# Kernel tuning notes

Hardware: AMD Instinct MI355X
Metric: run time of the kernel (lower is better)

The kernel has to match this reference:

```python
import jax, jax.numpy as jnp
import numpy as np

N_HEADS = 16
D_HEAD = 64
N_ROTATE = 32
ROPE_BASE = 10000.0
MAX_LEN = 2048  # round_up_to_multiple_of_256(keep count); static for jit
BATCH, SEQ = 2, 4096


def setup_inputs() -> dict:
    key = jax.random.key(0)
    kq, kk, kv = jax.random.split(key, 3)
    q = jax.random.normal(kq, (BATCH, N_HEADS, MAX_LEN, D_HEAD), jnp.float32)
    k = jax.random.normal(kk, (BATCH, N_HEADS, SEQ, D_HEAD), jnp.float32)
    v = jax.random.normal(kv, (BATCH, N_HEADS, SEQ, D_HEAD), jnp.float32)
    # causal full mask [batch, seq, seq] and full position ids [batch, seq]
    mask_full = jnp.broadcast_to(jnp.tril(jnp.ones((SEQ, SEQ), bool)), (BATCH, SEQ, SEQ))
    pos_full = jnp.broadcast_to(jnp.arange(SEQ, dtype=jnp.int32), (BATCH, SEQ))
    # skip_mask: exactly MAX_LEN kept tokens per row (random positions)
    rng = np.random.default_rng(0)
    sm = np.zeros((BATCH, SEQ), dtype=bool)
    for i in range(BATCH):
        sm[i, rng.permutation(SEQ)[:MAX_LEN]] = True
    return {"q": q, "k": k, "v": v, "mask_full": mask_full,
            "pos_full": pos_full, "skip_mask": jnp.asarray(sm)}


def _rope_rotate(x, pos):
    # x: [b, h, L, n_rotate], pos: [b, L]
    half = N_ROTATE // 2
    inv_freq = 1.0 / (ROPE_BASE ** (jnp.arange(0, N_ROTATE, 2, dtype=jnp.float32) / N_ROTATE))
    freqs = pos.astype(jnp.float32)[..., None] * inv_freq          # [b, L, half]
    emb = jnp.concatenate([freqs, freqs], axis=-1)[:, None]        # [b, 1, L, n_rotate]
    cos, sin = jnp.cos(emb), jnp.sin(emb)
    x1, x2 = x[..., :half], x[..., half:]
    rot = jnp.concatenate([-x2, x1], axis=-1)                      # rotate_half
    return x * cos + rot * sin


def reference(q, k, v, mask_full, pos_full, skip_mask):
    b, S = skip_mask.shape
    lengths = skip_mask.sum(axis=1)
    # vectorized _trim_attention_mask: stable argsort compacts kept indices to the front
    order = jnp.argsort(jnp.where(skip_mask, 0, 1), axis=1, stable=True)
    idx = order[:, :MAX_LEN]                                       # [b, max_len]
    brow = jnp.arange(b)[:, None]
    mask_trim = mask_full[brow, idx]                               # [b, max_len, S]
    pos_trim = pos_full[brow, idx]                                 # [b, max_len]
    valid = jnp.arange(MAX_LEN)[None, :] < lengths[:, None]
    mask_trim = mask_trim & valid[..., None]
    pos_trim = jnp.where(valid, pos_trim, 0)

    # partial RoPE on first n_rotate channels
    rq = _rope_rotate(q[..., :N_ROTATE], pos_trim)
    rk = _rope_rotate(k[..., :N_ROTATE], pos_full)
    q = jnp.concatenate([rq, q[..., N_ROTATE:]], axis=-1)
    k = jnp.concatenate([rk, k[..., N_ROTATE:]], axis=-1)

    # masked SDPA (bool mask broadcast over heads)
    scale = 1.0 / jnp.sqrt(jnp.float32(D_HEAD))
    scores = jnp.einsum('bhqd,bhkd->bhqk', q, k) * scale
    scores = jnp.where(mask_trim[:, None], scores, jnp.finfo(scores.dtype).min)
    attn = jax.nn.softmax(scores, axis=-1)
    return jnp.einsum('bhqk,bhkd->bhqd', attn, v)
```

## Files before the change

kernel.cpp:

```cpp
#include <hip/hip_runtime.h>
#include <math.h>

#define BB 2
#define HH 16
#define QQ 2048
#define SS 4096
#define DD 64
#define NRH 16
#define NQT 32

typedef unsigned short u16;
typedef unsigned int   u32;
typedef short bhalf8 __attribute__((ext_vector_type(8)));
typedef float f32x4  __attribute__((ext_vector_type(4)));

typedef __attribute__((address_space(1))) const u32 gu32;
typedef __attribute__((address_space(3))) u32 lu32;

#if __has_builtin(__builtin_amdgcn_exp2f)
#define EXP2(x) __builtin_amdgcn_exp2f(x)
#else
#define EXP2(x) exp2f(x)
#endif

union Frag16 { uint4 u; bhalf8 v; u16 s[8]; uint2 d[2]; };

__device__ __forceinline__ u16 f2bf(float f) {
  union { float f; u32 u; } c; c.f = f;
  return (u16)((c.u + 0x7FFFu + ((c.u >> 16) & 1u)) >> 16);
}

__device__ __forceinline__ u32 cvt_pk_bf16(float lo, float hi) {
  u32 r;
  asm("v_cvt_pk_bf16_f32 %0, %1, %2" : "=v"(r) : "v"(lo), "v"(hi));
  return r;
}

__device__ __forceinline__ bhalf8 ldfrag(const u16* p) {
  Frag16 f; f.u = *reinterpret_cast<const uint4*>(p); return f.v;
}

__device__ __forceinline__ void rope32(float* x, int pos) {
  const float step = 0.8304820237218405f;
  const float fp = (float)pos;
#pragma unroll
  for (int i = 0; i < NRH; ++i) {
    float ang = fp * exp2f(-step * (float)i);
    float sv, cv;
    __sincosf(ang, &sv, &cv);
    float a = x[i], b = x[i + NRH];
    x[i]       = a * cv - b * sv;
    x[i + NRH] = b * cv + a * sv;
  }
}

__global__ void prep_idx_kernel(const unsigned char* __restrict__ sm,
                                int* __restrict__ idx) {
  __shared__ int wsum[4];
  __shared__ int modes;
  const int tid = threadIdx.x;
  const int b = (int)blockIdx.x;

  int c = 0;
  for (int i = 0; i < 32; ++i) c += (sm[tid * 32 + i] != 0) ? 1 : 0;
#pragma unroll
  for (int off = 32; off; off >>= 1) c += __shfl_down(c, off);
  if ((tid & 63) == 0) wsum[tid >> 6] = c;
  __syncthreads();
  if (tid == 0) modes = (wsum[0] + wsum[1] + wsum[2] + wsum[3] > 3000) ? 1 : 0;
  __syncthreads();
  const bool byteMode = (modes != 0);
  const u32* sm32 = (const u32*)sm;

  const int base = b * SS + tid * 16;
  u32 flags = 0;
  for (int i = 0; i < 16; ++i) {
    bool f = byteMode ? (sm[base + i] != 0) : (sm32[base + i] != 0);
    flags |= ((u32)(f ? 1 : 0)) << i;
  }
  int cnt = __popc(flags);
  int vv = cnt;
#pragma unroll
  for (int off = 1; off < 64; off <<= 1) {
    int t = __shfl_up(vv, off);
    if ((tid & 63) >= off) vv += t;
  }
  __syncthreads();
  if ((tid & 63) == 63) wsum[tid >> 6] = vv;
  __syncthreads();
  int add = 0;
  for (int w2 = 0; w2 < (tid >> 6); ++w2) add += wsum[w2];
  int p = vv - cnt + add;
  for (int i = 0; i < 16; ++i) {
    if (flags & (1u << i)) {
      if (p < QQ) idx[b * QQ + p] = tid * 16 + i;
      ++p;
    }
  }
}

__global__ __launch_bounds__(256) void prep_kv_kernel(const float* __restrict__ k,
                                                      const float* __restrict__ v,
                                                      u16* __restrict__ kbf,
                                                      u16* __restrict__ vt) {
  __shared__ u16 tile[64][72];
  if (blockIdx.x < 512) {
    int r = blockIdx.x * 256 + threadIdx.x;
    int pos = r & (SS - 1);
    float x[64];
    const float4* src = (const float4*)(k + (size_t)r * DD);
#pragma unroll
    for (int i = 0; i < 16; ++i) {
      float4 t = src[i];
      x[4 * i] = t.x; x[4 * i + 1] = t.y; x[4 * i + 2] = t.z; x[4 * i + 3] = t.w;
    }
    rope32(x, pos);
    u16 tmp[64];
#pragma unroll
    for (int i = 0; i < 64; ++i) tmp[i] = f2bf(x[i]);
    uint4* dst = (uint4*)(kbf + (size_t)r * DD);
#pragma unroll
    for (int i = 0; i < 8; ++i) dst[i] = ((uint4*)tmp)[i];
  } else {
    int blk = (int)blockIdx.x - 512;
    int bh = blk >> 6;
    int jt = blk & 63;
    int t = threadIdx.x;
    int jl = t >> 2;
    int dc = (t & 3) * 16;
    const float4* src = (const float4*)(v + ((size_t)(bh * SS + jt * 64 + jl)) * DD + dc);
#pragma unroll
    for (int i = 0; i < 4; ++i) {
      float4 f = src[i];
      tile[jl][dc + 4 * i]     = f2bf(f.x);
      tile[jl][dc + 4 * i + 1] = f2bf(f.y);
      tile[jl][dc + 4 * i + 2] = f2bf(f.z);
      tile[jl][dc + 4 * i + 3] = f2bf(f.w);
    }
    __syncthreads();
    int d = t >> 2;
    int c = t & 3;
    u16 o[16];
#pragma unroll
    for (int m = 0; m < 16; ++m) {
      int p = c * 16 + m;
      int kp = (p & 32) | ((p & 4) << 2) | ((p >> 1) & 12) | (p & 3);
      o[m] = tile[kp][d];
    }
    uint4* dst = (uint4*)(vt + ((size_t)(bh * DD + d)) * SS + jt * 64 + c * 16);
    dst[0] = ((uint4*)o)[0];
    dst[1] = ((uint4*)o)[1];
  }
}

__device__ __forceinline__ void stage_tiles(const char* kb_bh, const char* vt_bh,
                                            u16* Kb, u16* Vb, int t0,
                                            int w, int srow, int schk) {
#pragma unroll
  for (int p2 = 0; p2 < 2; ++p2) {
    const int rr = w * 16 + p2 * 8 + srow;
    {
      const char* g = kb_bh + (size_t)(t0 + rr) * 128 + ((schk ^ (rr & 7)) * 16);
      lu32* l = (lu32*)((char*)Kb + (w * 16 + p2 * 8) * 128);
      __builtin_amdgcn_global_load_lds((gu32*)g, l, 16, 0, 0);
    }
    {
      const char* g = vt_bh + (size_t)rr * (SS * 2) + t0 * 2 + ((schk ^ (rr & 7)) * 16);
      lu32* l = (lu32*)((char*)Vb + (w * 16 + p2 * 8) * 128);
      __builtin_amdgcn_global_load_lds((gu32*)g, l, 16, 0, 0);
    }
  }
}

template <bool MASKED>
__device__ __forceinline__ void attn_tile(
    const u16* __restrict__ Kb, const u16* __restrict__ Vb,
    int t0, int grp, int col, int bnd,
    bhalf8 qa0, bhalf8 qa1,
    f32x4& acc0, f32x4& acc1, f32x4& acc2, f32x4& acc3,
    float& lsum) {
  const int swz = col & 7;
  f32x4 z = {0.f, 0.f, 0.f, 0.f};
  f32x4 s0 = z, s1 = z, s2 = z, s3 = z;
  {
    const u16* kr0 = Kb + (0 * 16 + col) * 64;
    const u16* kr1 = Kb + (1 * 16 + col) * 64;
    const u16* kr2 = Kb + (2 * 16 + col) * 64;
    const u16* kr3 = Kb + (3 * 16 + col) * 64;
    __builtin_amdgcn_s_setprio(1);
    bhalf8 a0 = ldfrag(kr0 + ((grp ^ swz) * 8));
    s0 = __builtin_amdgcn_mfma_f32_16x16x32_bf16(a0, qa0, s0, 0, 0, 0);
    bhalf8 b0 = ldfrag(kr0 + (((4 + grp) ^ swz) * 8));
    s0 = __builtin_amdgcn_mfma_f32_16x16x32_bf16(b0, qa1, s0, 0, 0, 0);
    bhalf8 a1 = ldfrag(kr1 + ((grp ^ swz) * 8));
    s1 = __builtin_amdgcn_mfma_f32_16x16x32_bf16(a1, qa0, s1, 0, 0, 0);
    bhalf8 b1 = ldfrag(kr1 + (((4 + grp) ^ swz) * 8));
    s1 = __builtin_amdgcn_mfma_f32_16x16x32_bf16(b1, qa1, s1, 0, 0, 0);
    bhalf8 a2 = ldfrag(kr2 + ((grp ^ swz) * 8));
    s2 = __builtin_amdgcn_mfma_f32_16x16x32_bf16(a2, qa0, s2, 0, 0, 0);
    bhalf8 b2 = ldfrag(kr2 + (((4 + grp) ^ swz) * 8));
    s2 = __builtin_amdgcn_mfma_f32_16x16x32_bf16(b2, qa1, s2, 0, 0, 0);
    bhalf8 a3 = ldfrag(kr3 + ((grp ^ swz) * 8));
    s3 = __builtin_amdgcn_mfma_f32_16x16x32_bf16(a3, qa0, s3, 0, 0, 0);
    bhalf8 b3 = ldfrag(kr3 + (((4 + grp) ^ swz) * 8));
    s3 = __builtin_amdgcn_mfma_f32_16x16x32_bf16(b3, qa1, s3, 0, 0, 0);
    __builtin_amdgcn_s_setprio(0);
  }

  uint2 w0, w1, w2, w3;
#define SM_C(SC, CB, W)                                                        \
  {                                                                            \
    float p0, p1, p2v, p3;                                                     \
    const int kb = t0 + (CB) + grp * 4;                                        \
    if (MASKED) {                                                              \
      p0  = (kb + 0 <= bnd) ? EXP2(SC[0] - 16.f) : 0.f;                        \
      p1  = (kb + 1 <= bnd) ? EXP2(SC[1] - 16.f) : 0.f;                        \
      p2v = (kb + 2 <= bnd) ? EXP2(SC[2] - 16.f) : 0.f;                        \
      p3  = (kb + 3 <= bnd) ? EXP2(SC[3] - 16.f) : 0.f;                        \
    } else {                                                                   \
      p0  = EXP2(SC[0] - 16.f);                                                \
      p1  = EXP2(SC[1] - 16.f);                                                \
      p2v = EXP2(SC[2] - 16.f);                                                \
      p3  = EXP2(SC[3] - 16.f);                                                \
    }                                                                          \
    lsum += (p0 + p1) + (p2v + p3);                                            \
    W.x = cvt_pk_bf16(p0, p1);                                                 \
    W.y = cvt_pk_bf16(p2v, p3);                                                \
  }
  SM_C(s0, 0,  w0)
  SM_C(s1, 16, w1)
  SM_C(s2, 32, w2)
  SM_C(s3, 48, w3)
#undef SM_C

  bhalf8 pv0, pv1;
  {
    Frag16 f0, f1;
    f0.d[0] = w0; f0.d[1] = w1;
    f1.d[0] = w2; f1.d[1] = w3;
    pv0 = f0.v; pv1 = f1.v;
  }

  {
    const u16* vr0 = Vb + (0  + col) * 64;
    const u16* vr1 = Vb + (16 + col) * 64;
    const u16* vr2 = Vb + (32 + col) * 64;
    const u16* vr3 = Vb + (48 + col) * 64;
    __builtin_amdgcn_s_setprio(1);
    bhalf8 x0 = ldfrag(vr0 + ((grp ^ swz) * 8));
    acc0 = __builtin_amdgcn_mfma_f32_16x16x32_bf16(x0, pv0, acc0, 0, 0, 0);
    bhalf8 y0 = ldfrag(vr0 + (((4 + grp) ^ swz) * 8));
    acc0 = __builtin_amdgcn_mfma_f32_16x16x32_bf16(y0, pv1, acc0, 0, 0, 0);
    bhalf8 x1 = ldfrag(vr1 + ((grp ^ swz) * 8));
    acc1 = __builtin_amdgcn_mfma_f32_16x16x32_bf16(x1, pv0, acc1, 0, 0, 0);
    bhalf8 y1 = ldfrag(vr1 + (((4 + grp) ^ swz) * 8));
    acc1 = __builtin_amdgcn_mfma_f32_16x16x32_bf16(y1, pv1, acc1, 0, 0, 0);
    bhalf8 x2 = ldfrag(vr2 + ((grp ^ swz) * 8));
    acc2 = __builtin_amdgcn_mfma_f32_16x16x32_bf16(x2, pv0, acc2, 0, 0, 0);
    bhalf8 y2 = ldfrag(vr2 + (((4 + grp) ^ swz) * 8));
    acc2 = __builtin_amdgcn_mfma_f32_16x16x32_bf16(y2, pv1, acc2, 0, 0, 0);
    bhalf8 x3 = ldfrag(vr3 + ((grp ^ swz) * 8));
    acc3 = __builtin_amdgcn_mfma_f32_16x16x32_bf16(x3, pv0, acc3, 0, 0, 0);
    bhalf8 y3 = ldfrag(vr3 + (((4 + grp) ^ swz) * 8));
    acc3 = __builtin_amdgcn_mfma_f32_16x16x32_bf16(y3, pv1, acc3, 0, 0, 0);
    __builtin_amdgcn_s_setprio(0);
  }
}

__global__ __launch_bounds__(256, 4) void attn_mfma_kernel(
    const float* __restrict__ qsrc, const u16* __restrict__ kbf,
    const u16* __restrict__ vt, const int* __restrict__ idx,
    float* __restrict__ out) {
  __shared__ u16 KbufA[64 * 64];
  __shared__ u16 VbufA[64 * 64];
  __shared__ u16 KbufB[64 * 64];
  __shared__ u16 VbufB[64 * 64];

  const int blk = (int)blockIdx.x;
  const int bh  = blk & 31;
  const int qt  = (NQT - 1) - (blk >> 5);
  const int q0  = qt * 64;
  const int b   = bh >> 4;
  const int tid  = threadIdx.x;
  const int w    = tid >> 6;
  const int lane = tid & 63;
  const int grp  = lane >> 4;
  const int col  = lane & 15;

  const char* kb_bh = (const char*)(kbf + (size_t)bh * SS * DD);
  const char* vt_bh = (const char*)(vt + (size_t)bh * DD * SS);

  const int srow = lane >> 3;
  const int schk = lane & 7;

  const int* idxb = idx + b * QQ + q0;
  const int bnd = idxb[w * 16 + col];
  const int wave_minb = idxb[w * 16];
  const int wave_maxb = idxb[w * 16 + 15];
  const int maxbound  = idxb[63];
  const int ntiles = (maxbound >> 6) + 1;

  bhalf8 qa0, qa1;
  {
    const int qrow = q0 + w * 16 + col;
    const float* qr = qsrc + (size_t)(bh * QQ + qrow) * DD;
    const int lof = (grp & 1) * 8;
    float4 A0 = *(const float4*)(qr + lof);
    float4 A1 = *(const float4*)(qr + lof + 4);
    float4 B0 = *(const float4*)(qr + 16 + lof);
    float4 B1 = *(const float4*)(qr + 16 + lof + 4);
    float4 C0 = *(const float4*)(qr + 32 + grp * 8);
    float4 C1 = *(const float4*)(qr + 32 + grp * 8 + 4);
    float xlo[8] = {A0.x, A0.y, A0.z, A0.w, A1.x, A1.y, A1.z, A1.w};
    float xhi[8] = {B0.x, B0.y, B0.z, B0.w, B1.x, B1.y, B1.z, B1.w};
    float xq1[8] = {C0.x, C0.y, C0.z, C0.w, C1.x, C1.y, C1.z, C1.w};
    const float scq = 0.125f * 1.44269504088896f;
    const float fp = (float)bnd;
    Frag16 f0, f1;
#pragma unroll
    for (int j = 0; j < 8; ++j) {
      float ang = fp * exp2f(-0.8304820237218405f * (float)(lof + j));
      float sv, cv;
      __sincosf(ang, &sv, &cv);
      float val = (grp >= 2) ? (xhi[j] * cv + xlo[j] * sv)
                             : (xlo[j] * cv - xhi[j] * sv);
      f0.s[j] = f2bf(val * scq);
      f1.s[j] = f2bf(xq1[j] * scq);
    }
    qa0 = f0.v; qa1 = f1.v;
  }

  f32x4 z = {0.f, 0.f, 0.f, 0.f};
  f32x4 acc0 = z, acc1 = z, acc2 = z, acc3 = z;
  float lsum = 0.f;

#define ATTN_CALL(M, KB, VB, T0)                                               \
  attn_tile<M>(KB, VB, T0, grp, col, bnd, qa0, qa1, acc0, acc1, acc2, acc3, lsum)

  stage_tiles(kb_bh, vt_bh, KbufA, VbufA, 0, w, srow, schk);
  __syncthreads();

  for (int ti = 0; ti < ntiles; ti += 2) {
    const bool has1 = (ti + 1) < ntiles;
    if (has1) stage_tiles(kb_bh, vt_bh, KbufB, VbufB, (ti + 1) << 6, w, srow, schk);
    {
      const int t0 = ti << 6;
      if (t0 <= wave_maxb) {
        if (t0 + 63 <= wave_minb) ATTN_CALL(false, KbufA, VbufA, t0);
        else                      ATTN_CALL(true,  KbufA, VbufA, t0);
      }
    }
    __syncthreads();
    if (has1) {
      if (ti + 2 < ntiles)
        stage_tiles(kb_bh, vt_bh, KbufA, VbufA, (ti + 2) << 6, w, srow, schk);
      {
        const int t0 = (ti + 1) << 6;
        if (t0 <= wave_maxb) {
          if (t0 + 63 <= wave_minb) ATTN_CALL(false, KbufB, VbufB, t0);
          else                      ATTN_CALL(true,  KbufB, VbufB, t0);
        }
      }
      __syncthreads();
    }
  }
#undef ATTN_CALL

  lsum += __shfl_xor(lsum, 16);
  lsum += __shfl_xor(lsum, 32);
  const float inv = 1.f / lsum;
  float* ob = out + (size_t)(bh * QQ + q0 + w * 16 + col) * DD + grp * 4;
  {
    float4 t;
    t.x = acc0[0] * inv; t.y = acc0[1] * inv; t.z = acc0[2] * inv; t.w = acc0[3] * inv;
    *(float4*)(ob + 0) = t;
    t.x = acc1[0] * inv; t.y = acc1[1] * inv; t.z = acc1[2] * inv; t.w = acc1[3] * inv;
    *(float4*)(ob + 16) = t;
    t.x = acc2[0] * inv; t.y = acc2[1] * inv; t.z = acc2[2] * inv; t.w = acc2[3] * inv;
    *(float4*)(ob + 32) = t;
    t.x = acc3[0] * inv; t.y = acc3[1] * inv; t.z = acc3[2] * inv; t.w = acc3[3] * inv;
    *(float4*)(ob + 48) = t;
  }
}

__global__ __launch_bounds__(64) void attn_fb_kernel(const float* __restrict__ q,
                                                     const float* __restrict__ ksrc,
                                                     const float* __restrict__ v,
                                                     const int* __restrict__ idx,
                                                     float* __restrict__ out) {
  int t = (int)(gridDim.x - 1u - blockIdx.x);
  int sub = t >> 5;
  int bh = t & 31;
  int b = bh >> 4;
  int lane = threadIdx.x;
  int qi = sub * 64 + lane;
  const int bound = idx[b * QQ + qi];

  float qreg[64];
  {
    const float4* qp = (const float4*)(q + ((size_t)bh * QQ + qi) * DD);
#pragma unroll
    for (int i = 0; i < 16; ++i) {
      float4 t4 = qp[i];
      qreg[4 * i] = t4.x; qreg[4 * i + 1] = t4.y;
      qreg[4 * i + 2] = t4.z; qreg[4 * i + 3] = t4.w;
    }
  }
  rope32(qreg, bound);
#pragma unroll
  for (int i = 0; i < 64; ++i) qreg[i] *= 0.125f;

  const float* kbase = ksrc + (size_t)bh * SS * DD;
  const float* vbase = v + (size_t)bh * SS * DD;
  float acc[64];
#pragma unroll
  for (int i = 0; i < 64; ++i) acc[i] = 0.f;
  float mrun = -INFINITY, lrun = 0.f;

  for (int j = 0; j <= bound; ++j) {
    float ka[64];
    const float4* kp = (const float4*)(kbase + (size_t)j * DD);
#pragma unroll
    for (int i = 0; i < 16; ++i) {
      float4 t4 = kp[i];
      ka[4 * i] = t4.x; ka[4 * i + 1] = t4.y;
      ka[4 * i + 2] = t4.z; ka[4 * i + 3] = t4.w;
    }
    rope32(ka, j);
    float s0 = 0.f, s1 = 0.f, s2 = 0.f, s3 = 0.f;
#pragma unroll
    for (int i = 0; i < 16; ++i) {
      s0 = fmaf(qreg[4 * i], ka[4 * i], s0);
      s1 = fmaf(qreg[4 * i + 1], ka[4 * i + 1], s1);
      s2 = fmaf(qreg[4 * i + 2], ka[4 * i + 2], s2);
      s3 = fmaf(qreg[4 * i + 3], ka[4 * i + 3], s3);
    }
    float sc = (s0 + s1) + (s2 + s3);
    if (sc > mrun) {
      float alpha = __expf(mrun - sc);
      lrun *= alpha;
#pragma unroll
      for (int i = 0; i < 64; ++i) acc[i] *= alpha;
      mrun = sc;
    }
    float pw = __expf(sc - mrun);
    lrun += pw;
    const float4* vp = (const float4*)(vbase + (size_t)j * DD);
#pragma unroll
    for (int i = 0; i < 16; ++i) {
      float4 t4 = vp[i];
      acc[4 * i] = fmaf(pw, t4.x, acc[4 * i]);
      acc[4 * i + 1] = fmaf(pw, t4.y, acc[4 * i + 1]);
      acc[4 * i + 2] = fmaf(pw, t4.z, acc[4 * i + 2]);
      acc[4 * i + 3] = fmaf(pw, t4.w, acc[4 * i + 3]);
    }
  }
  float inv = 1.0f / lrun;
  float4* op = (float4*)(out + ((size_t)bh * QQ + qi) * DD);
#pragma unroll
  for (int i = 0; i < 16; ++i) {
    float4 t4;
    t4.x = acc[4 * i] * inv; t4.y = acc[4 * i + 1] * inv;
    t4.z = acc[4 * i + 2] * inv; t4.w = acc[4 * i + 3] * inv;
    op[i] = t4;
  }
}

extern "C" void kernel_launch(void* const* d_in, const int* in_sizes, int n_in,
                              void* d_out, int out_size, void* d_ws, size_t ws_size,
                              hipStream_t stream) {
  (void)in_sizes; (void)n_in; (void)out_size;
  const float* q = (const float*)d_in[0];
  const float* k = (const float*)d_in[1];
  const float* v = (const float*)d_in[2];
  const unsigned char* skip = (const unsigned char*)d_in[5];
  float* out = (float*)d_out;

  char* base = (char*)d_ws;
  int* idx = (int*)base;
  const size_t kbytes = (size_t)BB * HH * SS * DD * 2;
  u16* kbf = (u16*)(base + 16384);
  u16* vtb = (u16*)(base + 16384 + kbytes);
  const size_t need = 16384 + 2 * kbytes;

  prep_idx_kernel<<<2, 256, 0, stream>>>(skip, idx);
  if (ws_size >= need) {
    prep_kv_kernel<<<512 + BB * HH * 64, 256, 0, stream>>>(k, v, kbf, vtb);
    attn_mfma_kernel<<<NQT * 32, 256, 0, stream>>>(q, kbf, vtb, idx, out);
  } else {
    attn_fb_kernel<<<1024, 64, 0, stream>>>(q, k, v, idx, out);
  }
}
```

Before: 288.4 us.

## Double query rows per wave to reuse K/V fragments across two query groups

```diff
diff --git a/kernel.cpp b/kernel.cpp
--- a/kernel.cpp
+++ b/kernel.cpp
@@ -7,7 +7,7 @@
 #define SS 4096
 #define DD 64
 #define NRH 16
-#define NQT 32
+#define NQT128 16
 
 typedef unsigned short u16;
 typedef unsigned int   u32;
@@ -175,13 +175,15 @@
 template <bool MASKED>
 __device__ __forceinline__ void attn_tile(
     const u16* __restrict__ Kb, const u16* __restrict__ Vb,
-    int t0, int grp, int col, int bnd,
-    bhalf8 qa0, bhalf8 qa1,
-    f32x4& acc0, f32x4& acc1, f32x4& acc2, f32x4& acc3,
-    float& lsum) {
+    int t0, int grp, int col, int bndA, int bndB,
+    bhalf8 qaA0, bhalf8 qaA1, bhalf8 qaB0, bhalf8 qaB1,
+    f32x4& accA0, f32x4& accA1, f32x4& accA2, f32x4& accA3,
+    f32x4& accB0, f32x4& accB1, f32x4& accB2, f32x4& accB3,
+    float& lsumA, float& lsumB) {
   const int swz = col & 7;
   f32x4 z = {0.f, 0.f, 0.f, 0.f};
-  f32x4 s0 = z, s1 = z, s2 = z, s3 = z;
+  f32x4 sA0 = z, sA1 = z, sA2 = z, sA3 = z;
+  f32x4 sB0 = z, sB1 = z, sB2 = z, sB3 = z;
   {
     const u16* kr0 = Kb + (0 * 16 + col) * 64;
     const u16* kr1 = Kb + (1 * 16 + col) * 64;
@@ -189,56 +191,70 @@
     const u16* kr3 = Kb + (3 * 16 + col) * 64;
     __builtin_amdgcn_s_setprio(1);
     bhalf8 a0 = ldfrag(kr0 + ((grp ^ swz) * 8));
-    s0 = __builtin_amdgcn_mfma_f32_16x16x32_bf16(a0, qa0, s0, 0, 0, 0);
+    sA0 = __builtin_amdgcn_mfma_f32_16x16x32_bf16(a0, qaA0, sA0, 0, 0, 0);
+    sB0 = __builtin_amdgcn_mfma_f32_16x16x32_bf16(a0, qaB0, sB0, 0, 0, 0);
     bhalf8 b0 = ldfrag(kr0 + (((4 + grp) ^ swz) * 8));
-    s0 = __builtin_amdgcn_mfma_f32_16x16x32_bf16(b0, qa1, s0, 0, 0, 0);
+    sA0 = __builtin_amdgcn_mfma_f32_16x16x32_bf16(b0, qaA1, sA0, 0, 0, 0);
+    sB0 = __builtin_amdgcn_mfma_f32_16x16x32_bf16(b0, qaB1, sB0, 0, 0, 0);
     bhalf8 a1 = ldfrag(kr1 + ((grp ^ swz) * 8));
-    s1 = __builtin_amdgcn_mfma_f32_16x16x32_bf16(a1, qa0, s1, 0, 0, 0);
+    sA1 = __builtin_amdgcn_mfma_f32_16x16x32_bf16(a1, qaA0, sA1, 0, 0, 0);
+    sB1 = __builtin_amdgcn_mfma_f32_16x16x32_bf16(a1, qaB0, sB1, 0, 0, 0);
     bhalf8 b1 = ldfrag(kr1 + (((4 + grp) ^ swz) * 8));
-    s1 = __builtin_amdgcn_mfma_f32_16x16x32_bf16(b1, qa1, s1, 0, 0, 0);
+    sA1 = __builtin_amdgcn_mfma_f32_16x16x32_bf16(b1, qaA1, sA1, 0, 0, 0);
+    sB1 = __builtin_amdgcn_mfma_f32_16x16x32_bf16(b1, qaB1, sB1, 0, 0, 0);
     bhalf8 a2 = ldfrag(kr2 + ((grp ^ swz) * 8));
-    s2 = __builtin_amdgcn_mfma_f32_16x16x32_bf16(a2, qa0, s2, 0, 0, 0);
+    sA2 = __builtin_amdgcn_mfma_f32_16x16x32_bf16(a2, qaA0, sA2, 0, 0, 0);
+    sB2 = __builtin_amdgcn_mfma_f32_16x16x32_bf16(a2, qaB0, sB2, 0, 0, 0);
     bhalf8 b2 = ldfrag(kr2 + (((4 + grp) ^ swz) * 8));
-    s2 = __builtin_amdgcn_mfma_f32_16x16x32_bf16(b2, qa1, s2, 0, 0, 0);
+    sA2 = __builtin_amdgcn_mfma_f32_16x16x32_bf16(b2, qaA1, sA2, 0, 0, 0);
+    sB2 = __builtin_amdgcn_mfma_f32_16x16x32_bf16(b2, qaB1, sB2, 0, 0, 0);
     bhalf8 a3 = ldfrag(kr3 + ((grp ^ swz) * 8));
-    s3 = __builtin_amdgcn_mfma_f32_16x16x32_bf16(a3, qa0, s3, 0, 0, 0);
+    sA3 = __builtin_amdgcn_mfma_f32_16x16x32_bf16(a3, qaA0, sA3, 0, 0, 0);
+    sB3 = __builtin_amdgcn_mfma_f32_16x16x32_bf16(a3, qaB0, sB3, 0, 0, 0);
     bhalf8 b3 = ldfrag(kr3 + (((4 + grp) ^ swz) * 8));
-    s3 = __builtin_amdgcn_mfma_f32_16x16x32_bf16(b3, qa1, s3, 0, 0, 0);
+    sA3 = __builtin_amdgcn_mfma_f32_16x16x32_bf16(b3, qaA1, sA3, 0, 0, 0);
+    sB3 = __builtin_amdgcn_mfma_f32_16x16x32_bf16(b3, qaB1, sB3, 0, 0, 0);
     __builtin_amdgcn_s_setprio(0);
   }
 
-  uint2 w0, w1, w2, w3;
-#define SM_C(SC, CB, W)                                                        \
+  uint2 wA0, wA1, wA2, wA3, wB0, wB1, wB2, wB3;
+#define SM_C(SC, CB, BND, LS, W)                                               \
   {                                                                            \
     float p0, p1, p2v, p3;                                                     \
     const int kb = t0 + (CB) + grp * 4;                                        \
     if (MASKED) {                                                              \
-      p0  = (kb + 0 <= bnd) ? EXP2(SC[0] - 16.f) : 0.f;                        \
-      p1  = (kb + 1 <= bnd) ? EXP2(SC[1] - 16.f) : 0.f;                        \
-      p2v = (kb + 2 <= bnd) ? EXP2(SC[2] - 16.f) : 0.f;                        \
-      p3  = (kb + 3 <= bnd) ? EXP2(SC[3] - 16.f) : 0.f;                        \
+      p0  = (kb + 0 <= (BND)) ? EXP2(SC[0] - 16.f) : 0.f;                      \
+      p1  = (kb + 1 <= (BND)) ? EXP2(SC[1] - 16.f) : 0.f;                      \
+      p2v = (kb + 2 <= (BND)) ? EXP2(SC[2] - 16.f) : 0.f;                      \
+      p3  = (kb + 3 <= (BND)) ? EXP2(SC[3] - 16.f) : 0.f;                      \
     } else {                                                                   \
       p0  = EXP2(SC[0] - 16.f);                                                \
       p1  = EXP2(SC[1] - 16.f);                                                \
       p2v = EXP2(SC[2] - 16.f);                                                \
       p3  = EXP2(SC[3] - 16.f);                                                \
     }                                                                          \
-    lsum += (p0 + p1) + (p2v + p3);                                            \
+    (LS) += (p0 + p1) + (p2v + p3);                                            \
     W.x = cvt_pk_bf16(p0, p1);                                                 \
     W.y = cvt_pk_bf16(p2v, p3);                                                \
   }
-  SM_C(s0, 0,  w0)
-  SM_C(s1, 16, w1)
-  SM_C(s2, 32, w2)
-  SM_C(s3, 48, w3)
+  SM_C(sA0, 0,  bndA, lsumA, wA0)
+  SM_C(sA1, 16, bndA, lsumA, wA1)
+  SM_C(sA2, 32, bndA, lsumA, wA2)
+  SM_C(sA3, 48, bndA, lsumA, wA3)
+  SM_C(sB0, 0,  bndB, lsumB, wB0)
+  SM_C(sB1, 16, bndB, lsumB, wB1)
+  SM_C(sB2, 32, bndB, lsumB, wB2)
+  SM_C(sB3, 48, bndB, lsumB, wB3)
 #undef SM_C
 
-  bhalf8 pv0, pv1;
-  {
-    Frag16 f0, f1;
-    f0.d[0] = w0; f0.d[1] = w1;
-    f1.d[0] = w2; f1.d[1] = w3;
-    pv0 = f0.v; pv1 = f1.v;
+  bhalf8 pvA0, pvA1, pvB0, pvB1;
+  {
+    Frag16 f0, f1, g0, g1;
+    f0.d[0] = wA0; f0.d[1] = wA1;
+    f1.d[0] = wA2; f1.d[1] = wA3;
+    g0.d[0] = wB0; g0.d[1] = wB1;
+    g1.d[0] = wB2; g1.d[1] = wB3;
+    pvA0 = f0.v; pvA1 = f1.v; pvB0 = g0.v; pvB1 = g1.v;
   }
 
   {
@@ -248,26 +264,34 @@
     const u16* vr3 = Vb + (48 + col) * 64;
     __builtin_amdgcn_s_setprio(1);
     bhalf8 x0 = ldfrag(vr0 + ((grp ^ swz) * 8));
-    acc0 = __builtin_amdgcn_mfma_f32_16x16x32_bf16(x0, pv0, acc0, 0, 0, 0);
+    accA0 = __builtin_amdgcn_mfma_f32_16x16x32_bf16(x0, pvA0, accA0, 0, 0, 0);
+    accB0 = __builtin_amdgcn_mfma_f32_16x16x32_bf16(x0, pvB0, accB0, 0, 0, 0);
     bhalf8 y0 = ldfrag(vr0 + (((4 + grp) ^ swz) * 8));
-    acc0 = __builtin_amdgcn_mfma_f32_16x16x32_bf16(y0, pv1, acc0, 0, 0, 0);
+    accA0 = __builtin_amdgcn_mfma_f32_16x16x32_bf16(y0, pvA1, accA0, 0, 0, 0);
+    accB0 = __builtin_amdgcn_mfma_f32_16x16x32_bf16(y0, pvB1, accB0, 0, 0, 0);
     bhalf8 x1 = ldfrag(vr1 + ((grp ^ swz) * 8));
-    acc1 = __builtin_amdgcn_mfma_f32_16x16x32_bf16(x1, pv0, acc1, 0, 0, 0);
+    accA1 = __builtin_amdgcn_mfma_f32_16x16x32_bf16(x1, pvA0, accA1, 0, 0, 0);
+    accB1 = __builtin_amdgcn_mfma_f32_16x16x32_bf16(x1, pvB0, accB1, 0, 0, 0);
     bhalf8 y1 = ldfrag(vr1 + (((4 + grp) ^ swz) * 8));
-    acc1 = __builtin_amdgcn_mfma_f32_16x16x32_bf16(y1, pv1, acc1, 0, 0, 0);
+    accA1 = __builtin_amdgcn_mfma_f32_16x16x32_bf16(y1, pvA1, accA1, 0, 0, 0);
+    accB1 = __builtin_amdgcn_mfma_f32_16x16x32_bf16(y1, pvB1, accB1, 0, 0, 0);
     bhalf8 x2 = ldfrag(vr2 + ((grp ^ swz) * 8));
-    acc2 = __builtin_amdgcn_mfma_f32_16x16x32_bf16(x2, pv0, acc2, 0, 0, 0);
+    accA2 = __builtin_amdgcn_mfma_f32_16x16x32_bf16(x2, pvA0, accA2, 0, 0, 0);
+    accB2 = __builtin_amdgcn_mfma_f32_16x16x32_bf16(x2, pvB0, accB2, 0, 0, 0);
     bhalf8 y2 = ldfrag(vr2 + (((4 + grp) ^ swz) * 8));
-    acc2 = __builtin_amdgcn_mfma_f32_16x16x32_bf16(y2, pv1, acc2, 0, 0, 0);
+    accA2 = __builtin_amdgcn_mfma_f32_16x16x32_bf16(y2, pvA1, accA2, 0, 0, 0);
+    accB2 = __builtin_amdgcn_mfma_f32_16x16x32_bf16(y2, pvB1, accB2, 0, 0, 0);
     bhalf8 x3 = ldfrag(vr3 + ((grp ^ swz) * 8));
-    acc3 = __builtin_amdgcn_mfma_f32_16x16x32_bf16(x3, pv0, acc3, 0, 0, 0);
+    accA3 = __builtin_amdgcn_mfma_f32_16x16x32_bf16(x3, pvA0, accA3, 0, 0, 0);
+    accB3 = __builtin_amdgcn_mfma_f32_16x16x32_bf16(x3, pvB0, accB3, 0, 0, 0);
     bhalf8 y3 = ldfrag(vr3 + (((4 + grp) ^ swz) * 8));
-    acc3 = __builtin_amdgcn_mfma_f32_16x16x32_bf16(y3, pv1, acc3, 0, 0, 0);
+    accA3 = __builtin_amdgcn_mfma_f32_16x16x32_bf16(y3, pvA1, accA3, 0, 0, 0);
+    accB3 = __builtin_amdgcn_mfma_f32_16x16x32_bf16(y3, pvB1, accB3, 0, 0, 0);
     __builtin_amdgcn_s_setprio(0);
   }
 }
 
-__global__ __launch_bounds__(256, 4) void attn_mfma_kernel(
+__global__ __launch_bounds__(256) void attn_mfma_kernel(
     const float* __restrict__ qsrc, const u16* __restrict__ kbf,
     const u16* __restrict__ vt, const int* __restrict__ idx,
     float* __restrict__ out) {
@@ -278,8 +302,9 @@
 
   const int blk = (int)blockIdx.x;
   const int bh  = blk & 31;
-  const int qt  = (NQT - 1) - (blk >> 5);
-  const int q0  = qt * 64;
+  const int rank = blk >> 5;
+  const int qt  = (rank < 8) ? (15 - 2 * rank) : (2 * (rank - 8));
+  const int q0  = qt * 128;
   const int b   = bh >> 4;
   const int tid  = threadIdx.x;
   const int w    = tid >> 6;
@@ -294,15 +319,16 @@
   const int schk = lane & 7;
 
   const int* idxb = idx + b * QQ + q0;
-  const int bnd = idxb[w * 16 + col];
-  const int wave_minb = idxb[w * 16];
-  const int wave_maxb = idxb[w * 16 + 15];
-  const int maxbound  = idxb[63];
+  const int bndA = idxb[w * 32 + col];
+  const int bndB = idxb[w * 32 + 16 + col];
+  const int wave_minb = idxb[w * 32];
+  const int wave_maxb = idxb[w * 32 + 31];
+  const int maxbound  = idxb[127];
   const int ntiles = (maxbound >> 6) + 1;
 
-  bhalf8 qa0, qa1;
-  {
-    const int qrow = q0 + w * 16 + col;
+  bhalf8 qaA0, qaA1, qaB0, qaB1;
+  {
+    const int qrow = q0 + w * 32 + col;
     const float* qr = qsrc + (size_t)(bh * QQ + qrow) * DD;
     const int lof = (grp & 1) * 8;
     float4 A0 = *(const float4*)(qr + lof);
@@ -315,7 +341,7 @@
     float xhi[8] = {B0.x, B0.y, B0.z, B0.w, B1.x, B1.y, B1.z, B1.w};
     float xq1[8] = {C0.x, C0.y, C0.z, C0.w, C1.x, C1.y, C1.z, C1.w};
     const float scq = 0.125f * 1.44269504088896f;
-    const float fp = (float)bnd;
+    const float fp = (float)bndA;
     Frag16 f0, f1;
 #pragma unroll
     for (int j = 0; j < 8; ++j) {
@@ -327,15 +353,46 @@
       f0.s[j] = f2bf(val * scq);
       f1.s[j] = f2bf(xq1[j] * scq);
     }
-    qa0 = f0.v; qa1 = f1.v;
+    qaA0 = f0.v; qaA1 = f1.v;
+  }
+  {
+    const int qrow = q0 + w * 32 + 16 + col;
+    const float* qr = qsrc + (size_t)(bh * QQ + qrow) * DD;
+    const int lof = (grp & 1) * 8;
+    float4 A0 = *(const float4*)(qr + lof);
+    float4 A1 = *(const float4*)(qr + lof + 4);
+    float4 B0 = *(const float4*)(qr + 16 + lof);
+    float4 B1 = *(const float4*)(qr + 16 + lof + 4);
+    float4 C0 = *(const float4*)(qr + 32 + grp * 8);
+    float4 C1 = *(const float4*)(qr + 32 + grp * 8 + 4);
+    float xlo[8] = {A0.x, A0.y, A0.z, A0.w, A1.x, A1.y, A1.z, A1.w};
+    float xhi[8] = {B0.x, B0.y, B0.z, B0.w, B1.x, B1.y, B1.z, B1.w};
+    float xq1[8] = {C0.x, C0.y, C0.z, C0.w, C1.x, C1.y, C1.z, C1.w};
+    const float scq = 0.125f * 1.44269504088896f;
+    const float fp = (float)bndB;
+    Frag16 f0, f1;
+#pragma unroll
+    for (int j = 0; j < 8; ++j) {
+      float ang = fp * exp2f(-0.8304820237218405f * (float)(lof + j));
+      float sv, cv;
+      __sincosf(ang, &sv, &cv);
+      float val = (grp >= 2) ? (xhi[j] * cv + xlo[j] * sv)
+                             : (xlo[j] * cv - xhi[j] * sv);
+      f0.s[j] = f2bf(val * scq);
+      f1.s[j] = f2bf(xq1[j] * scq);
+    }
+    qaB0 = f0.v; qaB1 = f1.v;
   }
 
   f32x4 z = {0.f, 0.f, 0.f, 0.f};
-  f32x4 acc0 = z, acc1 = z, acc2 = z, acc3 = z;
-  float lsum = 0.f;
+  f32x4 accA0 = z, accA1 = z, accA2 = z, accA3 = z;
+  f32x4 accB0 = z, accB1 = z, accB2 = z, accB3 = z;
+  float lsumA = 0.f, lsumB = 0.f;
 
 #define ATTN_CALL(M, KB, VB, T0)                                               \
-  attn_tile<M>(KB, VB, T0, grp, col, bnd, qa0, qa1, acc0, acc1, acc2, acc3, lsum)
+  attn_tile<M>(KB, VB, T0, grp, col, bndA, bndB, qaA0, qaA1, qaB0, qaB1,       \
+               accA0, accA1, accA2, accA3, accB0, accB1, accB2, accB3,         \
+               lsumA, lsumB)
 
   stage_tiles(kb_bh, vt_bh, KbufA, VbufA, 0, w, srow, schk);
   __syncthreads();
@@ -366,19 +423,34 @@
   }
 #undef ATTN_CALL
 
-  lsum += __shfl_xor(lsum, 16);
-  lsum += __shfl_xor(lsum, 32);
-  const float inv = 1.f / lsum;
-  float* ob = out + (size_t)(bh * QQ + q0 + w * 16 + col) * DD + grp * 4;
-  {
+  lsumA += __shfl_xor(lsumA, 16);
+  lsumA += __shfl_xor(lsumA, 32);
+  lsumB += __shfl_xor(lsumB, 16);
+  lsumB += __shfl_xor(lsumB, 32);
+  {
+    const float inv = 1.f / lsumA;
+    float* ob = out + (size_t)(bh * QQ + q0 + w * 32 + col) * DD + grp * 4;
     float4 t;
-    t.x = acc0[0] * inv; t.y = acc0[1] * inv; t.z = acc0[2] * inv; t.w = acc0[3] * inv;
+    t.x = accA0[0] * inv; t.y = accA0[1] * inv; t.z = accA0[2] * inv; t.w = accA0[3] * inv;
     *(float4*)(ob + 0) = t;
-    t.x = acc1[0] * inv; t.y = acc1[1] * inv; t.z = acc1[2] * inv; t.w = acc1[3] * inv;
+    t.x = accA1[0] * inv; t.y = accA1[1] * inv; t.z = accA1[2] * inv; t.w = accA1[3] * inv;
     *(float4*)(ob + 16) = t;
-    t.x = acc2[0] * inv; t.y = acc2[1] * inv; t.z = acc2[2] * inv; t.w = acc2[3] * inv;
+    t.x = accA2[0] * inv; t.y = accA2[1] * inv; t.z = accA2[2] * inv; t.w = accA2[3] * inv;
     *(float4*)(ob + 32) = t;
-    t.x = acc3[0] * inv; t.y = acc3[1] * inv; t.z = acc3[2] * inv; t.w = acc3[3] * inv;
+    t.x = accA3[0] * inv; t.y = accA3[1] * inv; t.z = accA3[2] * inv; t.w = accA3[3] * inv;
+    *(float4*)(ob + 48) = t;
+  }
+  {
+    const float inv = 1.f / lsumB;
+    float* ob = out + (size_t)(bh * QQ + q0 + w * 32 + 16 + col) * DD + grp * 4;
+    float4 t;
+    t.x = accB0[0] * inv; t.y = accB0[1] * inv; t.z = accB0[2] * inv; t.w = accB0[3] * inv;
+    *(float4*)(ob + 0) = t;
+    t.x = accB1[0] * inv; t.y = accB1[1] * inv; t.z = accB1[2] * inv; t.w = accB1[3] * inv;
+    *(float4*)(ob + 16) = t;
+    t.x = accB2[0] * inv; t.y = accB2[1] * inv; t.z = accB2[2] * inv; t.w = accB2[3] * inv;
+    *(float4*)(ob + 32) = t;
+    t.x = accB3[0] * inv; t.y = accB3[1] * inv; t.z = accB3[2] * inv; t.w = accB3[3] * inv;
     *(float4*)(ob + 48) = t;
   }
 }
@@ -486,7 +558,7 @@
   prep_idx_kernel<<<2, 256, 0, stream>>>(skip, idx);
   if (ws_size >= need) {
     prep_kv_kernel<<<512 + BB * HH * 64, 256, 0, stream>>>(k, v, kbf, vtb);
-    attn_mfma_kernel<<<NQT * 32, 256, 0, stream>>>(q, kbf, vtb, idx, out);
+    attn_mfma_kernel<<<NQT128 * 32, 256, 0, stream>>>(q, kbf, vtb, idx, out);
   } else {
     attn_fb_kernel<<<1024, 64, 0, stream>>>(q, k, v, idx, out);
   }
```

After: 297.9 us. 3.3% more time.
